# Kernel tuning notes

Measured on AMD Instinct MI355X. Metric: run time of the kernel, lower is better.

## Reference

```python
import jax, jax.numpy as jnp
import numpy as np

B = 64  # batch_size (number of graphs)


def _leaky(v):
    return jax.nn.leaky_relu(v, 0.01)


def _gine(x, src, dst, edge_attr, ew, eb, w1, b1, w2, b2):
    # GINEConv (eps=0): out = nn(x + sum_{j->i} relu(x_j + lin(edge_attr)))
    n = x.shape[0]
    msg = jax.nn.relu(x[src] + edge_attr @ ew + eb)      # [E, C]
    agg = jax.ops.segment_sum(msg, dst, num_segments=n)  # [N, C]
    h = x + agg
    h = _leaky(h @ w1 + b1)
    h = _leaky(h @ w2 + b2)
    return h


def setup_inputs() -> dict:
    key = jax.random.key(0)
    ks = jax.random.split(key, 32)
    N, E, NF, EF, H, A = 65536, 1048576, 32, 16, 128, 10
    s = 0.05
    inp = {
        'x': jax.random.normal(ks[0], (N, NF), jnp.float32),
        'edge_index': jax.random.randint(ks[1], (2, E), 0, N, jnp.int64)
        if jax.config.jax_enable_x64 else jax.random.randint(ks[1], (2, E), 0, N, jnp.int32),
        'edge_attr': jax.random.normal(ks[2], (E, EF), jnp.float32),
        'e1_w': jax.random.normal(ks[3], (EF, NF)) * s, 'e1_b': jnp.zeros((NF,)),
        'c1_w1': jax.random.normal(ks[4], (NF, H)) * s, 'c1_b1': jnp.zeros((H,)),
        'c1_w2': jax.random.normal(ks[5], (H, H)) * s, 'c1_b2': jnp.zeros((H,)),
        'e2_w': jax.random.normal(ks[6], (EF, H)) * s, 'e2_b': jnp.zeros((H,)),
        'c2_w1': jax.random.normal(ks[7], (H, H)) * s, 'c2_b1': jnp.zeros((H,)),
        'c2_w2': jax.random.normal(ks[8], (H, H)) * s, 'c2_b2': jnp.zeros((H,)),
        'a_w1': jax.random.normal(ks[9], (H, H)) * s, 'a_b1': jnp.zeros((H,)),
        'a_w2': jax.random.normal(ks[10], (H, A)) * s, 'a_b2': jnp.zeros((A,)),
        'n_w1': jax.random.normal(ks[11], (H, H)) * s, 'n_b1': jnp.zeros((H,)),
        'n_w2': jax.random.normal(ks[12], (H, H)) * s, 'n_b2': jnp.zeros((H,)),
        'n_w3': jax.random.normal(ks[13], (H, 1)) * s, 'n_b3': jnp.zeros((1,)),
    }
    return inp


def reference(x, edge_index, edge_attr,
              e1_w, e1_b, c1_w1, c1_b1, c1_w2, c1_b2,
              e2_w, e2_b, c2_w1, c2_b1, c2_w2, c2_b2,
              a_w1, a_b1, a_w2, a_b2,
              n_w1, n_b1, n_w2, n_b2, n_w3, n_b3):
    src, dst = edge_index[0], edge_index[1]
    h = _gine(x, src, dst, edge_attr, e1_w, e1_b, c1_w1, c1_b1, c1_w2, c1_b2)
    h = jax.nn.relu(h)  # dropout is identity in eval mode
    h = _gine(h, src, dst, edge_attr, e2_w, e2_b, c2_w1, c2_b1, c2_w2, c2_b2)
    H = h.shape[-1]
    hb = h.reshape(B, -1, H)            # [B, Nper, H]
    pooled = hb.mean(axis=1)            # [B, H]
    a = _leaky(_leaky(pooled @ a_w1 + a_b1) @ a_w2 + a_b2)
    action_prob = jax.nn.softmax(a, axis=1)
    # reinterpret flat node order as [Nper, B, H], as in the torch reshape
    xr = h.reshape(-1, B, H)
    nh = _leaky(xr @ n_w1 + n_b1)
    nh = _leaky(nh @ n_w2 + n_b2)
    node_scores = jax.nn.sigmoid(nh @ n_w3 + n_b3)[..., 0].T  # [B, Nper]
    return action_prob, node_scores
```

## Files before the change

### kernel.cpp

```cpp
#include <hip/hip_runtime.h>
#include <math.h>

#define NNODES 65536
#define NEDGES 1048576
#define NF 32
#define EF 16
#define HD 128
#define NACT 10
#define NB 64
#define NPER 1024

typedef unsigned short u16;
typedef float  vf4  __attribute__((ext_vector_type(4)));
typedef __bf16 vbf8 __attribute__((ext_vector_type(8)));
#define BC8(v) __builtin_bit_cast(vbf8, v)

__device__ __forceinline__ float leakyf(float v) { return v > 0.0f ? v : 0.01f * v; }

__device__ __forceinline__ u16 f2bf(float x) {
    unsigned u = __float_as_uint(x);
    return (u16)((u + 0x7FFFu + ((u >> 16) & 1u)) >> 16);
}
__device__ __forceinline__ float bf2f(u16 h) { return __uint_as_float(((unsigned)h) << 16); }

__device__ __forceinline__ void cvt4(const float4 s, uint2& hi, uint2& lo) {
    const u16 h0 = f2bf(s.x), h1 = f2bf(s.y), h2 = f2bf(s.z), h3 = f2bf(s.w);
    hi = make_uint2((unsigned)h0 | ((unsigned)h1 << 16), (unsigned)h2 | ((unsigned)h3 << 16));
    const u16 l0 = f2bf(s.x - bf2f(h0)), l1 = f2bf(s.y - bf2f(h1));
    const u16 l2 = f2bf(s.z - bf2f(h2)), l3 = f2bf(s.w - bf2f(h3));
    lo = make_uint2((unsigned)l0 | ((unsigned)l1 << 16), (unsigned)l2 | ((unsigned)l3 << 16));
}

__global__ __launch_bounds__(256) void hist_kernel(const int* __restrict__ ei, int* __restrict__ cnt)
{
    const int i = blockIdx.x * 256 + threadIdx.x;
    if (i < NEDGES) atomicAdd(&cnt[ei[NEDGES + i]], 1);
}

__global__ __launch_bounds__(1024) void scan_kernel(const int* __restrict__ cnt, int* __restrict__ rs)
{
    __shared__ int s[1024];
    const int t = threadIdx.x;
    int loc[64];
    int tot = 0;
    const int4* c4 = (const int4*)(cnt + t * 64);
    #pragma unroll
    for (int j = 0; j < 16; ++j) {
        const int4 v = c4[j];
        loc[4*j+0] = v.x; loc[4*j+1] = v.y; loc[4*j+2] = v.z; loc[4*j+3] = v.w;
        tot += v.x + v.y + v.z + v.w;
    }
    s[t] = tot;
    __syncthreads();
    for (int off = 1; off < 1024; off <<= 1) {
        const int v = (t >= off) ? s[t - off] : 0;
        __syncthreads();
        s[t] += v;
        __syncthreads();
    }
    int run = s[t] - tot;
    #pragma unroll
    for (int j = 0; j < 64; ++j) { rs[t * 64 + j] = run; run += loc[j]; }
    if (t == 0) rs[NNODES] = NEDGES;
}

__global__ __launch_bounds__(256) void scatter_kernel(
    const int* __restrict__ ei, const float* __restrict__ ea,
    const int* __restrict__ rs, int* __restrict__ fill,
    int* __restrict__ ssrc, float* __restrict__ sea)
{
    const int i = blockIdx.x * 256 + threadIdx.x;
    if (i < NEDGES) {
        const int d = ei[NEDGES + i];
        const int pos = rs[d] + atomicAdd(&fill[d], 1);
        ssrc[pos] = ei[i];
        const float4* s4 = (const float4*)ea + (size_t)i * 4;
        float4*       d4 = (float4*)sea + (size_t)pos * 4;
        d4[0] = s4[0]; d4[1] = s4[1]; d4[2] = s4[2]; d4[3] = s4[3];
    }
}

__global__ __launch_bounds__(256) void pack_w_kernel(
    const float* __restrict__ W, int KB, u16* __restrict__ hi, u16* __restrict__ lo)
{
    const int t = blockIdx.x * 256 + threadIdx.x;
    const int j = t & 7, lane = (t >> 3) & 63, rest = t >> 9;
    const int kb = rest % KB, fb = rest / KB;
    if (fb >= 8) return;
    const int k = kb * 32 + (lane >> 4) * 8 + j;
    const int f = fb * 16 + (lane & 15);
    const float val = W[k * HD + f];
    const u16 h = f2bf(val);
    hi[t] = h;
    lo[t] = f2bf(val - bf2f(h));
}

__global__ __launch_bounds__(256) void e1_agg_kernel(
    const float* __restrict__ x, const int* __restrict__ rs,
    const int* __restrict__ ssrc, const float* __restrict__ sea,
    const float* __restrict__ w, const float* __restrict__ b, float* __restrict__ agg)
{
    const int tid  = threadIdx.x;
    const int lane = tid & 63;
    const int f    = lane & 31;
    const int half = lane >> 5;
    const int node = blockIdx.x * 4 + (tid >> 6);
    float wr[EF];
    #pragma unroll
    for (int k = 0; k < EF; ++k) wr[k] = w[k * NF + f];
    const float bf = b[f];
    const int beg = rs[node], end = rs[node + 1];
    float acc = 0.0f;
    int e = beg + half;
    for (; e + 2 < end; e += 4) {
        const int sA = ssrc[e], sB = ssrc[e + 2];
        const float4* pA = (const float4*)sea + (size_t)e * 4;
        const float4* pB = (const float4*)sea + (size_t)(e + 2) * 4;
        const float4 A0 = pA[0], A1 = pA[1], A2 = pA[2], A3 = pA[3];
        const float4 B0 = pB[0], B1 = pB[1], B2 = pB[2], B3 = pB[3];
        const float xA = x[(size_t)sA * NF + f];
        const float xB = x[(size_t)sB * NF + f];
        float evA[EF] = {A0.x,A0.y,A0.z,A0.w, A1.x,A1.y,A1.z,A1.w,
                         A2.x,A2.y,A2.z,A2.w, A3.x,A3.y,A3.z,A3.w};
        float evB[EF] = {B0.x,B0.y,B0.z,B0.w, B1.x,B1.y,B1.z,B1.w,
                         B2.x,B2.y,B2.z,B2.w, B3.x,B3.y,B3.z,B3.w};
        float mA = bf, mB = bf;
        #pragma unroll
        for (int k = 0; k < EF; ++k) {
            mA = fmaf(evA[k], wr[k], mA);
            mB = fmaf(evB[k], wr[k], mB);
        }
        acc += fmaxf(xA + mA, 0.0f) + fmaxf(xB + mB, 0.0f);
    }
    for (; e < end; e += 2) {
        const int sA = ssrc[e];
        const float4* pA = (const float4*)sea + (size_t)e * 4;
        const float4 A0 = pA[0], A1 = pA[1], A2 = pA[2], A3 = pA[3];
        float evA[EF] = {A0.x,A0.y,A0.z,A0.w, A1.x,A1.y,A1.z,A1.w,
                         A2.x,A2.y,A2.z,A2.w, A3.x,A3.y,A3.z,A3.w};
        float mA = bf;
        #pragma unroll
        for (int k = 0; k < EF; ++k) mA = fmaf(evA[k], wr[k], mA);
        acc += fmaxf(x[(size_t)sA * NF + f] + mA, 0.0f);
    }
    acc += __shfl_xor(acc, 32, 64);
    if (half == 0) agg[(size_t)node * NF + f] = acc;
}

__global__ __launch_bounds__(256) void e2_agg_kernel(
    const float* __restrict__ h, const int* __restrict__ rs,
    const int* __restrict__ ssrc, const float* __restrict__ sea,
    const float* __restrict__ w, const float* __restrict__ b, float* __restrict__ agg)
{
    const int tid  = threadIdx.x;
    const int lane = tid & 63;
    const int f    = lane * 2;
    const int node = blockIdx.x * 4 + (tid >> 6);
    float wr0[EF], wr1[EF];
    #pragma unroll
    for (int k = 0; k < EF; ++k) { wr0[k] = w[k * HD + f]; wr1[k] = w[k * HD + f + 1]; }
    const float b0 = b[f], b1 = b[f + 1];
    const int beg = __builtin_amdgcn_readfirstlane(rs[node]);
    const int end = __builtin_amdgcn_readfirstlane(rs[node + 1]);
    float acc0 = 0.0f, acc1 = 0.0f;
    int e = beg;
    for (; e + 2 <= end; e += 2) {
        const int sA = ssrc[e];
        const int sB = ssrc[e + 1];
        const float2 hA = *(const float2*)&h[(size_t)sA * HD + f];
        const float2 hB = *(const float2*)&h[(size_t)sB * HD + f];
        const float* aA = &sea[(size_t)e * EF];
        const float* aB = aA + EF;
        float mA0 = b0, mA1 = b1, mB0 = b0, mB1 = b1;
        #pragma unroll
        for (int k = 0; k < EF; ++k) {
            const float vA = aA[k];
            const float vB = aB[k];
            mA0 = fmaf(vA, wr0[k], mA0);
            mA1 = fmaf(vA, wr1[k], mA1);
            mB0 = fmaf(vB, wr0[k], mB0);
            mB1 = fmaf(vB, wr1[k], mB1);
        }
        acc0 += fmaxf(hA.x + mA0, 0.0f) + fmaxf(hB.x + mB0, 0.0f);
        acc1 += fmaxf(hA.y + mA1, 0.0f) + fmaxf(hB.y + mB1, 0.0f);
    }
    if (e < end) {
        const int sA = ssrc[e];
        const float2 hA = *(const float2*)&h[(size_t)sA * HD + f];
        const float* aA = &sea[(size_t)e * EF];
        float mA0 = b0, mA1 = b1;
        #pragma unroll
        for (int k = 0; k < EF; ++k) {
            const float vA = aA[k];
            mA0 = fmaf(vA, wr0[k], mA0);
            mA1 = fmaf(vA, wr1[k], mA1);
        }
        acc0 += fmaxf(hA.x + mA0, 0.0f);
        acc1 += fmaxf(hA.y + mA1, 0.0f);
    }
    *(float2*)&agg[(size_t)node * HD + f] = make_float2(acc0, acc1);
}


#define ROW128 272
#define ROW32  80

__device__ __forceinline__ void mfma_layer128(
    const unsigned char* __restrict__ aH, const unsigned char* __restrict__ aL,
    const u16* __restrict__ wH, const u16* __restrict__ wL,
    const float* __restrict__ bias, int lane, vf4* __restrict__ acc)
{
    const int quad = lane >> 4, fm = lane & 15;
    int4 Bh[4], Bl[4];
    #pragma unroll
    for (int kb = 0; kb < 4; ++kb) {
        Bh[kb] = *(const int4*)(aH + fm * ROW128 + kb * 64 + quad * 16);
        Bl[kb] = *(const int4*)(aL + fm * ROW128 + kb * 64 + quad * 16);
    }
    #pragma unroll
    for (int fb = 0; fb < 8; ++fb) {
        const float4 bv = *(const float4*)&bias[fb * 16 + quad * 4];
        vf4 a = {bv.x, bv.y, bv.z, bv.w};
        #pragma unroll
        for (int kb = 0; kb < 4; ++kb) {
            const int4 wh = *(const int4*)(wH + ((fb * 4 + kb) * 64 + lane) * 8);
            const int4 wl = *(const int4*)(wL + ((fb * 4 + kb) * 64 + lane) * 8);
            a = __builtin_amdgcn_mfma_f32_16x16x32_bf16(BC8(wh), BC8(Bl[kb]), a, 0, 0, 0);
            a = __builtin_amdgcn_mfma_f32_16x16x32_bf16(BC8(wl), BC8(Bh[kb]), a, 0, 0, 0);
            a = __builtin_amdgcn_mfma_f32_16x16x32_bf16(BC8(wh), BC8(Bh[kb]), a, 0, 0, 0);
        }
        acc[fb] = a;
    }
}

__device__ __forceinline__ void mfma_layer32(
    const unsigned char* __restrict__ aH, const unsigned char* __restrict__ aL,
    const u16* __restrict__ wH, const u16* __restrict__ wL,
    const float* __restrict__ bias, int lane, vf4* __restrict__ acc)
{
    const int quad = lane >> 4, fm = lane & 15;
    const int4 Bh = *(const int4*)(aH + fm * ROW32 + quad * 16);
    const int4 Bl = *(const int4*)(aL + fm * ROW32 + quad * 16);
    #pragma unroll
    for (int fb = 0; fb < 8; ++fb) {
        const float4 bv = *(const float4*)&bias[fb * 16 + quad * 4];
        vf4 a = {bv.x, bv.y, bv.z, bv.w};
        const int4 wh = *(const int4*)(wH + (fb * 64 + lane) * 8);
        const int4 wl = *(const int4*)(wL + (fb * 64 + lane) * 8);
        a = __builtin_amdgcn_mfma_f32_16x16x32_bf16(BC8(wh), BC8(Bl), a, 0, 0, 0);
        a = __builtin_amdgcn_mfma_f32_16x16x32_bf16(BC8(wl), BC8(Bh), a, 0, 0, 0);
        a = __builtin_amdgcn_mfma_f32_16x16x32_bf16(BC8(wh), BC8(Bh), a, 0, 0, 0);
        acc[fb] = a;
    }
}

__device__ __forceinline__ void store_act_leaky(
    unsigned char* __restrict__ aH, unsigned char* __restrict__ aL, int lane, vf4* __restrict__ acc)
{
    const int quad = lane >> 4, fm = lane & 15;
    #pragma unroll
    for (int fb = 0; fb < 8; ++fb) {
        const float4 s = {leakyf(acc[fb][0]), leakyf(acc[fb][1]), leakyf(acc[fb][2]), leakyf(acc[fb][3])};
        acc[fb][0] = s.x; acc[fb][1] = s.y; acc[fb][2] = s.z; acc[fb][3] = s.w;
        uint2 phi, plo;
        cvt4(s, phi, plo);
        *(uint2*)(aH + fm * ROW128 + fb * 32 + quad * 8) = phi;
        *(uint2*)(aL + fm * ROW128 + fb * 32 + quad * 8) = plo;
    }
}

__global__ __launch_bounds__(256) void n1_kernel(
    const float* __restrict__ x, const float* __restrict__ agg,
    const u16* __restrict__ w1h, const u16* __restrict__ w1l, const float* __restrict__ b1,
    const u16* __restrict__ w2h, const u16* __restrict__ w2l, const float* __restrict__ b2,
    float* __restrict__ hout)
{
    __shared__ __align__(16) unsigned char smem[4][2560 + 2 * 16 * ROW128];
    const int tid = threadIdx.x, lane = tid & 63, wid = tid >> 6;
    const int quad = lane >> 4, fm = lane & 15;
    const int tile = blockIdx.x * 4 + wid;
    unsigned char* inH = smem[wid];
    unsigned char* inL = inH + 16 * ROW32;
    unsigned char* aH  = inH + 2560;
    unsigned char* aL  = aH + 16 * ROW128;
    const size_t base = (size_t)tile * 16 * NF;
    #pragma unroll
    for (int i = 0; i < 2; ++i) {
        const int flat = i * 64 + lane;
        const int node = flat >> 3, kq = flat & 7;
        const float4 xv = *(const float4*)&x[base + node * NF + kq * 4];
        const float4 av = *(const float4*)&agg[base + node * NF + kq * 4];
        const float4 s = {xv.x + av.x, xv.y + av.y, xv.z + av.z, xv.w + av.w};
        uint2 phi, plo;
        cvt4(s, phi, plo);
        *(uint2*)(inH + node * ROW32 + kq * 8) = phi;
        *(uint2*)(inL + node * ROW32 + kq * 8) = plo;
    }
    __syncthreads();
    vf4 acc[8];
    mfma_layer32(inH, inL, w1h, w1l, b1, lane, acc);
    __syncthreads();
    store_act_leaky(aH, aL, lane, acc);
    __syncthreads();
    mfma_layer128(aH, aL, w2h, w2l, b2, lane, acc);
    const size_t ob = (size_t)tile * 16 * HD;
    #pragma unroll
    for (int fb = 0; fb < 8; ++fb) {
        const float4 o = {fmaxf(acc[fb][0], 0.0f), fmaxf(acc[fb][1], 0.0f),
                          fmaxf(acc[fb][2], 0.0f), fmaxf(acc[fb][3], 0.0f)};
        *(float4*)&hout[ob + fm * HD + fb * 16 + quad * 4] = o;
    }
}

__global__ __launch_bounds__(256) void n2_kernel(
    const float* __restrict__ h, const float* __restrict__ agg,
    const u16* __restrict__ w1h, const u16* __restrict__ w1l, const float* __restrict__ b1,
    const u16* __restrict__ w2h, const u16* __restrict__ w2l, const float* __restrict__ b2,
    const u16* __restrict__ m1h, const u16* __restrict__ m1l, const float* __restrict__ nb1,
    const u16* __restrict__ m2h, const u16* __restrict__ m2l, const float* __restrict__ nb2,
    const float* __restrict__ nw3, const float* __restrict__ nb3,
    float* __restrict__ pooled, float* __restrict__ scores)
{
    __shared__ __align__(16) unsigned char smem[4][2 * 16 * ROW128];
    const int tid = threadIdx.x, lane = tid & 63, wid = tid >> 6;
    const int quad = lane >> 4, fm = lane & 15;
    const int tile = blockIdx.x * 4 + wid;
    unsigned char* aH = smem[wid];
    unsigned char* aL = aH + 16 * ROW128;
    const size_t base = (size_t)tile * 16 * HD;
    #pragma unroll
    for (int i = 0; i < 8; ++i) {
        const int flat = i * 64 + lane;
        const int node = flat >> 5, kq = flat & 31;
        const float4 hv = *(const float4*)&h[base + node * HD + kq * 4];
        const float4 av = *(const float4*)&agg[base + node * HD + kq * 4];
        const float4 s = {hv.x + av.x, hv.y + av.y, hv.z + av.z, hv.w + av.w};
        uint2 phi, plo;
        cvt4(s, phi, plo);
        *(uint2*)(aH + node * ROW128 + kq * 8) = phi;
        *(uint2*)(aL + node * ROW128 + kq * 8) = plo;
    }
    __syncthreads();
    vf4 acc[8];
    mfma_layer128(aH, aL, w1h, w1l, b1, lane, acc);
    __syncthreads();
    store_act_leaky(aH, aL, lane, acc);
    __syncthreads();
    mfma_layer128(aH, aL, w2h, w2l, b2, lane, acc);
    __syncthreads();
    store_act_leaky(aH, aL, lane, acc);
    {
        const int g = tile >> 6;
        #pragma unroll
        for (int fb = 0; fb < 8; ++fb) {
            vf4 t = acc[fb];
            #pragma unroll
            for (int off = 1; off < 16; off <<= 1) {
                t[0] += __shfl_xor(t[0], off, 64);
                t[1] += __shfl_xor(t[1], off, 64);
                t[2] += __shfl_xor(t[2], off, 64);
                t[3] += __shfl_xor(t[3], off, 64);
            }
            #pragma unroll
            for (int r = 0; r < 4; ++r) {
                const int item = fb * 4 + r;
                if (fm == (item >> 1))
                    atomicAdd(&pooled[g * HD + fb * 16 + quad * 4 + r], t[r]);
            }
        }
    }
    __syncthreads();
    mfma_layer128(aH, aL, m1h, m1l, nb1, lane, acc);
    __syncthreads();
    store_act_leaky(aH, aL, lane, acc);
    __syncthreads();
    mfma_layer128(aH, aL, m2h, m2l, nb2, lane, acc);
    float v = 0.0f;
    #pragma unroll
    for (int fb = 0; fb < 8; ++fb) {
        const float4 w3v = *(const float4*)&nw3[fb * 16 + quad * 4];
        v += leakyf(acc[fb][0]) * w3v.x + leakyf(acc[fb][1]) * w3v.y
           + leakyf(acc[fb][2]) * w3v.z + leakyf(acc[fb][3]) * w3v.w;
    }
    v += __shfl_xor(v, 16, 64);
    v += __shfl_xor(v, 32, 64);
    if (lane < 16) {
        const int node = tile * 16 + fm;
        const float s = v + nb3[0];
        scores[(node & 63) * NPER + (node >> 6)] = 1.0f / (1.0f + expf(-s));
    }
}

__global__ __launch_bounds__(128) void act_kernel(
    const float* __restrict__ pooled,
    const float* __restrict__ w1, const float* __restrict__ b1,
    const float* __restrict__ w2, const float* __restrict__ b2,
    float* __restrict__ out)
{
    __shared__ __align__(16) float p[HD];
    __shared__ float a1[HD];
    __shared__ float z[NACT];
    __shared__ float red2[2];
    const int g = blockIdx.x;
    const int tid = threadIdx.x;
    p[tid] = pooled[g * HD + tid] * (1.0f / NPER);
    __syncthreads();
    float acc = b1[tid];
    for (int k = 0; k < HD; ++k) acc = fmaf(p[k], w1[k * HD + tid], acc);
    a1[tid] = leakyf(acc);
    __syncthreads();
    if (tid < NACT) {
        float a2 = b2[tid];
        for (int k = 0; k < HD; ++k) a2 = fmaf(a1[k], w2[k * NACT + tid], a2);
        z[tid] = leakyf(a2);
    }
    __syncthreads();
    if (tid == 0) {
        float m = z[0];
        for (int i = 1; i < NACT; ++i) m = fmaxf(m, z[i]);
        red2[0] = m;
    }
    __syncthreads();
    if (tid < NACT) z[tid] = expf(z[tid] - red2[0]);
    __syncthreads();
    if (tid == 0) {
        float s = 0.0f;
        for (int i = 0; i < NACT; ++i) s += z[i];
        red2[1] = s;
    }
    __syncthreads();
    if (tid < NACT) out[g * NACT + tid] = z[tid] / red2[1];
}

extern "C" void kernel_launch(void* const* d_in, const int* in_sizes, int n_in,
                              void* d_out, int out_size, void* d_ws, size_t ws_size,
                              hipStream_t stream)
{
    const float* x    = (const float*)d_in[0];
    const int*   ei   = (const int*)d_in[1];
    const float* ea   = (const float*)d_in[2];
    const float* e1w  = (const float*)d_in[3];
    const float* e1b  = (const float*)d_in[4];
    const float* c1w1 = (const float*)d_in[5];
    const float* c1b1 = (const float*)d_in[6];
    const float* c1w2 = (const float*)d_in[7];
    const float* c1b2 = (const float*)d_in[8];
    const float* e2w  = (const float*)d_in[9];
    const float* e2b  = (const float*)d_in[10];
    const float* c2w1 = (const float*)d_in[11];
    const float* c2b1 = (const float*)d_in[12];
    const float* c2w2 = (const float*)d_in[13];
    const float* c2b2 = (const float*)d_in[14];
    const float* aw1  = (const float*)d_in[15];
    const float* ab1  = (const float*)d_in[16];
    const float* aw2  = (const float*)d_in[17];
    const float* ab2  = (const float*)d_in[18];
    const float* nw1  = (const float*)d_in[19];
    const float* nb1  = (const float*)d_in[20];
    const float* nw2  = (const float*)d_in[21];
    const float* nb2  = (const float*)d_in[22];
    const float* nw3  = (const float*)d_in[23];
    const float* nb3  = (const float*)d_in[24];

    float* out = (float*)d_out;
    char*  ws  = (char*)d_ws;
    const size_t MB = 1024 * 1024;
    float* h      = (float*)(ws);
    float* agg2   = (float*)(ws + 32  * MB);
    float* sea    = (float*)(ws + 64  * MB);
    float* agg1   = (float*)(ws + 128 * MB);
    float* pooled = (float*)(ws + 136 * MB);
    u16*   pw     = (u16*)  (ws + 136 * MB + 64 * 1024);
    int*   cnt    = (int*)  (ws + 137 * MB);
    int*   fill   = (int*)  (ws + 138 * MB);
    int*   rs     = (int*)  (ws + 139 * MB);
    int*   ssrc   = (int*)  (ws + 140 * MB);

    u16* p_c1w1 = pw;
    u16* p_c1w2 = pw + 1 * 32768;
    u16* p_c2w1 = pw + 2 * 32768;
    u16* p_c2w2 = pw + 3 * 32768;
    u16* p_nw1  = pw + 4 * 32768;
    u16* p_nw2  = pw + 5 * 32768;

    hipMemsetAsync(cnt,    0, NNODES * sizeof(int), stream);
    hipMemsetAsync(fill,   0, NNODES * sizeof(int), stream);
    hipMemsetAsync(pooled, 0, (size_t)NB * HD * sizeof(float), stream);

    pack_w_kernel<<<16,  256, 0, stream>>>(c1w1, 1, p_c1w1, p_c1w1 + 16384);
    pack_w_kernel<<<64,  256, 0, stream>>>(c1w2, 4, p_c1w2, p_c1w2 + 16384);
    pack_w_kernel<<<64,  256, 0, stream>>>(c2w1, 4, p_c2w1, p_c2w1 + 16384);
    pack_w_kernel<<<64,  256, 0, stream>>>(c2w2, 4, p_c2w2, p_c2w2 + 16384);
    pack_w_kernel<<<64,  256, 0, stream>>>(nw1,  4, p_nw1,  p_nw1  + 16384);
    pack_w_kernel<<<64,  256, 0, stream>>>(nw2,  4, p_nw2,  p_nw2  + 16384);

    hist_kernel<<<NEDGES / 256, 256, 0, stream>>>(ei, cnt);
    scan_kernel<<<1, 1024, 0, stream>>>(cnt, rs);
    scatter_kernel<<<NEDGES / 256, 256, 0, stream>>>(ei, ea, rs, fill, ssrc, sea);

    e1_agg_kernel<<<NNODES / 4, 256, 0, stream>>>(x, rs, ssrc, sea, e1w, e1b, agg1);
    n1_kernel<<<NNODES / 64, 256, 0, stream>>>(x, agg1,
                                               p_c1w1, p_c1w1 + 16384, c1b1,
                                               p_c1w2, p_c1w2 + 16384, c1b2, h);
    e2_agg_kernel<<<NNODES / 4, 256, 0, stream>>>(h, rs, ssrc, sea, e2w, e2b, agg2);
    n2_kernel<<<NNODES / 64, 256, 0, stream>>>(h, agg2,
                                               p_c2w1, p_c2w1 + 16384, c2b1,
                                               p_c2w2, p_c2w2 + 16384, c2b2,
                                               p_nw1,  p_nw1  + 16384, nb1,
                                               p_nw2,  p_nw2  + 16384, nb2,
                                               nw3, nb3, pooled, out + NB * NACT);
    act_kernel<<<NB, 128, 0, stream>>>(pooled, aw1, ab1, aw2, ab2, out);
}
```

Baseline: 591.2 us.

## Split edge-attr scatter into index scatter plus coalesced gather; batch weight packing

The scatter kernel now writes only the source index and the original edge id to the CSR position. A separate permute kernel gathers edge attributes with coalesced writes (four threads per edge, one float4 each), replacing the scattered 64-byte writes. The six weight-packing launches are merged into one kernel, and the two memsets are combined by placing fill right after cnt. This adds one extra pass over the index array and one more kernel launch, and it reuses agg2's workspace region for seidx.

```diff
diff --git a/kernel.cpp b/kernel.cpp
--- a/kernel.cpp
+++ b/kernel.cpp
@@ -65,25 +65,41 @@
 }
 
 __global__ __launch_bounds__(256) void scatter_kernel(
-    const int* __restrict__ ei, const float* __restrict__ ea,
-    const int* __restrict__ rs, int* __restrict__ fill,
-    int* __restrict__ ssrc, float* __restrict__ sea)
+    const int* __restrict__ ei, const int* __restrict__ rs, int* __restrict__ fill,
+    int* __restrict__ ssrc, int* __restrict__ seidx)
 {
     const int i = blockIdx.x * 256 + threadIdx.x;
     if (i < NEDGES) {
         const int d = ei[NEDGES + i];
         const int pos = rs[d] + atomicAdd(&fill[d], 1);
-        ssrc[pos] = ei[i];
-        const float4* s4 = (const float4*)ea + (size_t)i * 4;
-        float4*       d4 = (float4*)sea + (size_t)pos * 4;
-        d4[0] = s4[0]; d4[1] = s4[1]; d4[2] = s4[2]; d4[3] = s4[3];
-    }
-}
-
-__global__ __launch_bounds__(256) void pack_w_kernel(
-    const float* __restrict__ W, int KB, u16* __restrict__ hi, u16* __restrict__ lo)
+        ssrc[pos]  = ei[i];
+        seidx[pos] = i;
+    }
+}
+
+__global__ __launch_bounds__(256) void permute_kernel(
+    const int* __restrict__ seidx, const float* __restrict__ ea, float* __restrict__ sea)
 {
     const int t = blockIdx.x * 256 + threadIdx.x;
+    const int e = t >> 2, part = t & 3;
+    const int idx = seidx[e];
+    ((float4*)sea)[(size_t)e * 4 + part] = ((const float4*)ea)[(size_t)idx * 4 + part];
+}
+
+__global__ __launch_bounds__(256) void pack_all_kernel(
+    const float* __restrict__ w0, const float* __restrict__ w1, const float* __restrict__ w2,
+    const float* __restrict__ w3, const float* __restrict__ w4, const float* __restrict__ w5,
+    u16* __restrict__ pw)
+{
+    const int bid = blockIdx.x;
+    const float* W; int KB, seg, sbase;
+    if (bid < 16) { W = w0; KB = 1; seg = 0; sbase = 0; }
+    else {
+        const int i = (bid - 16) >> 6;
+        seg = i + 1; sbase = 16 + i * 64; KB = 4;
+        W = (i == 0) ? w1 : (i == 1) ? w2 : (i == 2) ? w3 : (i == 3) ? w4 : w5;
+    }
+    const int t = (bid - sbase) * 256 + threadIdx.x;
     const int j = t & 7, lane = (t >> 3) & 63, rest = t >> 9;
     const int kb = rest % KB, fb = rest / KB;
     if (fb >= 8) return;
@@ -91,8 +107,9 @@
     const int f = fb * 16 + (lane & 15);
     const float val = W[k * HD + f];
     const u16 h = f2bf(val);
-    hi[t] = h;
-    lo[t] = f2bf(val - bf2f(h));
+    u16* dst = pw + seg * 32768;
+    dst[t] = h;
+    dst[16384 + t] = f2bf(val - bf2f(h));
 }
 
 __global__ __launch_bounds__(256) void e1_agg_kernel(
@@ -201,7 +218,6 @@
     *(float2*)&agg[(size_t)node * HD + f] = make_float2(acc0, acc1);
 }
 
-
 #define ROW128 272
 #define ROW32  80
 
@@ -467,12 +483,13 @@
     const size_t MB = 1024 * 1024;
     float* h      = (float*)(ws);
     float* agg2   = (float*)(ws + 32  * MB);
+    int*   seidx  = (int*)  (ws + 32  * MB);
     float* sea    = (float*)(ws + 64  * MB);
     float* agg1   = (float*)(ws + 128 * MB);
     float* pooled = (float*)(ws + 136 * MB);
     u16*   pw     = (u16*)  (ws + 136 * MB + 64 * 1024);
     int*   cnt    = (int*)  (ws + 137 * MB);
-    int*   fill   = (int*)  (ws + 138 * MB);
+    int*   fill   = (int*)  (ws + 137 * MB + 256 * 1024);
     int*   rs     = (int*)  (ws + 139 * MB);
     int*   ssrc   = (int*)  (ws + 140 * MB);
 
@@ -483,20 +500,15 @@
     u16* p_nw1  = pw + 4 * 32768;
     u16* p_nw2  = pw + 5 * 32768;
 
-    hipMemsetAsync(cnt,    0, NNODES * sizeof(int), stream);
-    hipMemsetAsync(fill,   0, NNODES * sizeof(int), stream);
+    hipMemsetAsync(cnt,    0, 2 * NNODES * sizeof(int), stream);
     hipMemsetAsync(pooled, 0, (size_t)NB * HD * sizeof(float), stream);
 
-    pack_w_kernel<<<16,  256, 0, stream>>>(c1w1, 1, p_c1w1, p_c1w1 + 16384);
-    pack_w_kernel<<<64,  256, 0, stream>>>(c1w2, 4, p_c1w2, p_c1w2 + 16384);
-    pack_w_kernel<<<64,  256, 0, stream>>>(c2w1, 4, p_c2w1, p_c2w1 + 16384);
-    pack_w_kernel<<<64,  256, 0, stream>>>(c2w2, 4, p_c2w2, p_c2w2 + 16384);
-    pack_w_kernel<<<64,  256, 0, stream>>>(nw1,  4, p_nw1,  p_nw1  + 16384);
-    pack_w_kernel<<<64,  256, 0, stream>>>(nw2,  4, p_nw2,  p_nw2  + 16384);
+    pack_all_kernel<<<336, 256, 0, stream>>>(c1w1, c1w2, c2w1, c2w2, nw1, nw2, pw);
 
     hist_kernel<<<NEDGES / 256, 256, 0, stream>>>(ei, cnt);
     scan_kernel<<<1, 1024, 0, stream>>>(cnt, rs);
-    scatter_kernel<<<NEDGES / 256, 256, 0, stream>>>(ei, ea, rs, fill, ssrc, sea);
+    scatter_kernel<<<NEDGES / 256, 256, 0, stream>>>(ei, rs, fill, ssrc, seidx);
+    permute_kernel<<<NEDGES / 64, 256, 0, stream>>>(seidx, ea, sea);
 
     e1_agg_kernel<<<NNODES / 4, 256, 0, stream>>>(x, rs, ssrc, sea, e1w, e1b, agg1);
     n1_kernel<<<NNODES / 64, 256, 0, stream>>>(x, agg1,
```

Result: no change. 581.8 us (-1.6%).
